# Optimization experiments

Hardware: AMD Instinct MI355X
Metric: run time of the kernel (lower is better)

The kernel has to match this reference:

```python
import jax, jax.numpy as jnp
import numpy as np
from jax import lax

H = 16        # linear_num_key_heads == linear_num_value_heads
DK = 64       # linear_key_head_dim
DV = 128      # linear_value_head_dim
HID = 2048    # hidden_size
KCONV = 4     # linear_conv_kernel_dim
SEQ = 2048
KEY_DIM = H * DK       # 1024
VAL_DIM = H * DV       # 2048
CONV_DIM = 2 * KEY_DIM + VAL_DIM  # 4096


def _l2norm(x, eps=1e-6):
    return x * lax.rsqrt(jnp.sum(x * x, axis=-1, keepdims=True) + eps)


def setup_inputs() -> dict:
    key = jax.random.key(0)
    ks = jax.random.split(key, 10)
    s = 0.02
    return {
        "hidden_states": jax.random.normal(ks[0], (1, SEQ, HID), jnp.float32),
        "in_proj_qkv": jax.random.normal(ks[1], (CONV_DIM, HID), jnp.float32) * s,
        "in_proj_a": jax.random.normal(ks[2], (H, HID), jnp.float32) * s,
        "in_proj_b": jax.random.normal(ks[3], (H, HID), jnp.float32) * s,
        "in_proj_z": jax.random.normal(ks[4], (VAL_DIM, HID), jnp.float32) * s,
        "conv_w": jax.random.normal(ks[5], (CONV_DIM, 1, KCONV), jnp.float32) * 0.5,
        "A_log": jax.random.normal(ks[6], (H,), jnp.float32) * 0.5,
        "dt_bias": jnp.ones((H,), jnp.float32),
        "norm_w": jnp.ones((DV,), jnp.float32),
        "out_proj": jax.random.normal(ks[7], (HID, VAL_DIM), jnp.float32) * s,
        "is_prefill": 1,
    }


def reference(hidden_states, in_proj_qkv, in_proj_a, in_proj_b, in_proj_z,
              conv_w, A_log, dt_bias, norm_w, out_proj, is_prefill):
    b, s, _ = hidden_states.shape  # b == 1
    # QKV projection: (1, S, CONV_DIM)
    mixed = jnp.einsum('bsh,oh->bso', hidden_states, in_proj_qkv)
    # Depthwise causal conv1d over time (left pad K-1), then SiLU
    x = mixed.transpose(0, 2, 1)  # (1, C, S)
    x = lax.conv_general_dilated(
        x, conv_w, window_strides=(1,), padding=[(KCONV - 1, 0)],
        feature_group_count=CONV_DIM, dimension_numbers=('NCH', 'OIH', 'NCH'))
    mixed = jax.nn.silu(x).transpose(0, 2, 1)[0]  # (S, CONV_DIM), squeeze batch

    q = mixed[:, :KEY_DIM].reshape(s, H, DK)
    k = mixed[:, KEY_DIM:2 * KEY_DIM].reshape(s, H, DK)
    v = mixed[:, 2 * KEY_DIM:].reshape(s, H, DV)

    hs = hidden_states[0]  # (S, HID)
    a = hs @ in_proj_a.T                      # (S, H)
    g = -jnp.exp(A_log) * jax.nn.softplus(a + dt_bias)  # (S, H) log-decay
    beta = jax.nn.sigmoid(hs @ in_proj_b.T)   # (S, H)
    z = (hs @ in_proj_z.T).reshape(s, H, DV)  # (S, H, DV)

    q = _l2norm(q) * (1.0 / np.sqrt(DK))
    k = _l2norm(k)

    # Delta-rule recurrence; prefill -> zero initial state
    S0 = jnp.zeros((H, DK, DV), jnp.float32)

    def step(St, inp):
        q_t, k_t, v_t, g_t, beta_t = inp
        St = St * jnp.exp(g_t)[:, None, None]            # decay
        kv_mem = jnp.einsum('hk,hkv->hv', k_t, St)       # read
        delta = (v_t - kv_mem) * beta_t[:, None]         # gated error
        St = St + jnp.einsum('hk,hv->hkv', k_t, delta)   # rank-1 update
        o_t = jnp.einsum('hk,hkv->hv', q_t, St)          # query read
        return St, o_t

    _, core = lax.scan(step, S0, (q, k, v, g, beta))  # core: (S, H, DV)

    # Gated RMSNorm over DV, then SiLU(z) gate
    var = jnp.mean(core * core, axis=-1, keepdims=True)
    core = core * lax.rsqrt(var + 1e-6) * norm_w
    core = core * jax.nn.silu(z)
    core = core.reshape(1, s, VAL_DIM)
    return jnp.einsum('bsv,hv->bsh', core, out_proj)
```

## Files before the change

kernel.cpp:

```cpp
#include <hip/hip_runtime.h>
#include <stdint.h>


#define SEQ 2048
#define HIDDEN 2048
#define NH 16
#define DKv 64
#define DVv 128
#define KEY_DIM 1024
#define VAL_DIM 2048
#define CONV_DIM 4096

typedef __bf16 bf16;
typedef unsigned short u16;
typedef __attribute__((ext_vector_type(8))) __bf16 bf16x8;
typedef __attribute__((ext_vector_type(4))) __bf16 bf16x4;
typedef __attribute__((ext_vector_type(4))) float f32x4;

#define AS1 __attribute__((address_space(1)))
#define AS3 __attribute__((address_space(3)))
#define GLDS16(src, dst) __builtin_amdgcn_global_load_lds((AS1 const void*)(src), (AS3 void*)(dst), 16, 0, 0)

__device__ __forceinline__ float b2f(u16 u) {
  union { unsigned int i; float f; } c; c.i = ((unsigned int)u) << 16; return c.f;
}
__device__ __forceinline__ float sigmoidf_(float x) { return 1.0f / (1.0f + __expf(-x)); }

__global__ void detect_dtype(const u16* __restrict__ p, unsigned* __restrict__ flag) {
  int lane = threadIdx.x;
  int cnt = 0;
  for (int w = lane; w < 2048; w += 64) {
    unsigned e = (p[2 * w] >> 7) & 0xFF;
    if (e < 64) cnt++;
  }
  cnt += __shfl_xor(cnt, 1);  cnt += __shfl_xor(cnt, 2);  cnt += __shfl_xor(cnt, 4);
  cnt += __shfl_xor(cnt, 8);  cnt += __shfl_xor(cnt, 16); cnt += __shfl_xor(cnt, 32);
  if (lane == 0) *flag = (cnt > 64) ? 1u : 0u;
}

__global__ __launch_bounds__(256)
void cvt_bf16(const void* __restrict__ src, bf16* __restrict__ dst, long n,
              const unsigned* __restrict__ flagp) {
  long i = ((long)blockIdx.x * 256 + threadIdx.x) * 8;
  if (i >= n) return;
  if (*flagp) {
    const f32x4* s = (const f32x4*)((const float*)src + i);
    f32x4 a = s[0], b = s[1];
    bf16x8 o;
#pragma unroll
    for (int j = 0; j < 4; ++j) { o[j] = (bf16)a[j]; o[4 + j] = (bf16)b[j]; }
    *(bf16x8*)(dst + i) = o;
  } else {
    *(bf16x8*)(dst + i) = *(const bf16x8*)((const bf16*)src + i);
  }
}

template<bool F32OUT>
__global__ __launch_bounds__(256, 2)
void gemm_nt(const void* __restrict__ Araw, const void* __restrict__ Braw,
             void* __restrict__ Cv, int N, int K,
             const unsigned* __restrict__ flagp, int useA, int useB) {
  __shared__ __align__(16) bf16 As[128 * 32];
  __shared__ __align__(16) bf16 Bs[128 * 32];
  const bool f32g = (*flagp != 0);
  const bool fA = useA && f32g;
  const bool fB = useB && f32g;
  const int tid  = threadIdx.x;
  const int lane = tid & 63;
  const int wv   = tid >> 6;
  const int wm   = (wv & 1) << 6;
  const int wn   = (wv >> 1) << 6;
  const long bm  = (long)blockIdx.y * 128;
  const long bn  = (long)blockIdx.x * 128;

  f32x4 acc[4][4] = {};

  for (int k0 = 0; k0 < K; k0 += 32) {
#pragma unroll
    for (int it = 0; it < 2; ++it) {
      int e   = (it * 256 + tid) * 8;
      int row = e >> 5;
      int col = e & 31;
      long offA = (bm + row) * (long)K + (k0 + col);
      long offB = (bn + row) * (long)K + (k0 + col);
      if (fA) {
        const float* g = (const float*)Araw + offA;
        f32x4 u0 = *(const f32x4*)g, u1 = *(const f32x4*)(g + 4);
        bf16x8 bv;
#pragma unroll
        for (int j = 0; j < 4; ++j) { bv[j] = (bf16)u0[j]; bv[4 + j] = (bf16)u1[j]; }
        *(bf16x8*)&As[e] = bv;
      } else {
        const bf16* g = (const bf16*)Araw + offA;
        GLDS16(g, &As[e]);
      }
      if (fB) {
        const float* g = (const float*)Braw + offB;
        f32x4 u0 = *(const f32x4*)g, u1 = *(const f32x4*)(g + 4);
        bf16x8 bv;
#pragma unroll
        for (int j = 0; j < 4; ++j) { bv[j] = (bf16)u0[j]; bv[4 + j] = (bf16)u1[j]; }
        *(bf16x8*)&Bs[e] = bv;
      } else {
        const bf16* g = (const bf16*)Braw + offB;
        GLDS16(g, &Bs[e]);
      }
    }
    __syncthreads();

    const bf16x8* As8 = (const bf16x8*)As;
    const bf16x8* Bs8 = (const bf16x8*)Bs;
    const int r = lane & 15, q = lane >> 4;
    bf16x8 af[4], bfr[4];
#pragma unroll
    for (int i = 0; i < 4; ++i) af[i]  = As8[(wm + i * 16 + r) * 4 + q];
#pragma unroll
    for (int j = 0; j < 4; ++j) bfr[j] = Bs8[(wn + j * 16 + r) * 4 + q];
#pragma unroll
    for (int i = 0; i < 4; ++i)
#pragma unroll
      for (int j = 0; j < 4; ++j)
        acc[i][j] = __builtin_amdgcn_mfma_f32_16x16x32_bf16(af[i], bfr[j], acc[i][j], 0, 0, 0);
    __syncthreads();
  }

  const int r = lane & 15, q = lane >> 4;
#pragma unroll
  for (int i = 0; i < 4; ++i)
#pragma unroll
    for (int j = 0; j < 4; ++j) {
      long row = bm + wm + i * 16 + q * 4;
      long col = bn + wn + j * 16 + r;
#pragma unroll
      for (int rr = 0; rr < 4; ++rr) {
        if constexpr (F32OUT) ((float*)Cv)[(row + rr) * N + col] = acc[i][j][rr];
        else                  ((bf16*)Cv)[(row + rr) * N + col] = (bf16)acc[i][j][rr];
      }
    }
}

__device__ void gemm_body_bf16(char* smemc, const bf16* __restrict__ A,
                               const bf16* __restrict__ B, bf16* __restrict__ C,
                               int N, int K, int bx, int by, int tid) {
  bf16* As = (bf16*)smemc;
  bf16* Bs = (bf16*)(smemc + 8192);
  const int lane = tid & 63;
  const int wv = tid >> 6, wm = (wv & 1) << 6, wn = (wv >> 1) << 6;
  const long bm = (long)by * 128, bn = (long)bx * 128;
  f32x4 acc[4][4] = {};
  for (int k0 = 0; k0 < K; k0 += 32) {
#pragma unroll
    for (int it = 0; it < 2; ++it) {
      int e = (it * 256 + tid) * 8;
      int row = e >> 5, col = e & 31;
      const bf16* gA = A + (bm + row) * (long)K + k0 + col;
      const bf16* gB = B + (bn + row) * (long)K + k0 + col;
      GLDS16(gA, &As[e]);
      GLDS16(gB, &Bs[e]);
    }
    __syncthreads();
    const bf16x8* As8 = (const bf16x8*)As;
    const bf16x8* Bs8 = (const bf16x8*)Bs;
    const int r = lane & 15, q = lane >> 4;
    bf16x8 af[4], bfr[4];
#pragma unroll
    for (int i = 0; i < 4; ++i) af[i]  = As8[(wm + i * 16 + r) * 4 + q];
#pragma unroll
    for (int j = 0; j < 4; ++j) bfr[j] = Bs8[(wn + j * 16 + r) * 4 + q];
#pragma unroll
    for (int i = 0; i < 4; ++i)
#pragma unroll
      for (int j = 0; j < 4; ++j)
        acc[i][j] = __builtin_amdgcn_mfma_f32_16x16x32_bf16(af[i], bfr[j], acc[i][j], 0, 0, 0);
    __syncthreads();
  }
  const int r = lane & 15, q = lane >> 4;
#pragma unroll
  for (int i = 0; i < 4; ++i)
#pragma unroll
    for (int j = 0; j < 4; ++j) {
      long row = bm + wm + i * 16 + q * 4;
      long col = bn + wn + j * 16 + r;
#pragma unroll
      for (int rr = 0; rr < 4; ++rr)
        C[(row + rr) * (long)N + col] = (bf16)acc[i][j][rr];
    }
}

__global__ __launch_bounds__(256)
void proj_ab(const void* __restrict__ hsr, const void* __restrict__ War,
             const void* __restrict__ Wbr, const void* __restrict__ A_logr,
             const void* __restrict__ dtbr,
             float* __restrict__ eg, float* __restrict__ bet,
             float* __restrict__ gb,
             const unsigned* __restrict__ flagp) {
  const bool f32g = (*flagp != 0);
  const int t  = threadIdx.x;
  const int sl = t >> 5;
  const int o  = t & 31;
  const int h  = o & 15;
  const long s = (long)blockIdx.x * 8 + sl;
  float a0 = 0.f, a1 = 0.f, a2 = 0.f, a3 = 0.f;
  if (f32g) {
    const f32x4* x4 = (const f32x4*)((const float*)hsr + s * HIDDEN);
    const f32x4* w4 = (const f32x4*)((const float*)((o < 16) ? War : Wbr) + (long)h * HIDDEN);
#pragma unroll 8
    for (int k4 = 0; k4 < 512; ++k4) {
      f32x4 xv = x4[k4], wv = w4[k4];
      a0 = fmaf(xv[0], wv[0], a0);
      a1 = fmaf(xv[1], wv[1], a1);
      a2 = fmaf(xv[2], wv[2], a2);
      a3 = fmaf(xv[3], wv[3], a3);
    }
  } else {
    const bf16x8* x8 = (const bf16x8*)((const bf16*)hsr + s * HIDDEN);
    const bf16x8* w8 = (const bf16x8*)((const bf16*)((o < 16) ? War : Wbr) + (long)h * HIDDEN);
#pragma unroll 8
    for (int k8 = 0; k8 < 256; ++k8) {
      bf16x8 xv = x8[k8], wv = w8[k8];
      a0 += (float)xv[0] * (float)wv[0] + (float)xv[4] * (float)wv[4];
      a1 += (float)xv[1] * (float)wv[1] + (float)xv[5] * (float)wv[5];
      a2 += (float)xv[2] * (float)wv[2] + (float)xv[6] * (float)wv[6];
      a3 += (float)xv[3] * (float)wv[3] + (float)xv[7] * (float)wv[7];
    }
  }
  const float a = (a0 + a1) + (a2 + a3);
  if (o < 16) {
    float alog = f32g ? ((const float*)A_logr)[h] : b2f(((const u16*)A_logr)[h]);
    float dtb  = f32g ? ((const float*)dtbr)[h]   : b2f(((const u16*)dtbr)[h]);
    float xx = a + dtb;
    float sp = fmaxf(xx, 0.f) + log1pf(__expf(-fabsf(xx)));
    float gg = -__expf(alog) * sp;
    if (gb) gb[s * NH + h] = gg;
    eg[s * NH + h] = __expf(gg);
  } else {
    bet[s * NH + h] = sigmoidf_(a);
  }
}

__global__ __launch_bounds__(256)
void conv_norm(const bf16* __restrict__ mixed, const void* __restrict__ convwr,
               bf16* __restrict__ qbuf, bf16* __restrict__ kbuf, bf16* __restrict__ vbuf,
               const unsigned* __restrict__ flagp) {
  const bool f32g = (*flagp != 0);
  const int s = blockIdx.x;
  const int c = blockIdx.y * 256 + threadIdx.x;
  float w0, w1, w2, w3;
  if (f32g) {
    const float* wp = (const float*)convwr + (long)c * 4;
    w0 = wp[0]; w1 = wp[1]; w2 = wp[2]; w3 = wp[3];
  } else {
    const u16* wp = (const u16*)convwr + (long)c * 4;
    w0 = b2f(wp[0]); w1 = b2f(wp[1]); w2 = b2f(wp[2]); w3 = b2f(wp[3]);
  }
  float acc = w3 * (float)mixed[(long)s * CONV_DIM + c];
  if (s >= 1) acc += w2 * (float)mixed[(long)(s - 1) * CONV_DIM + c];
  if (s >= 2) acc += w1 * (float)mixed[(long)(s - 2) * CONV_DIM + c];
  if (s >= 3) acc += w0 * (float)mixed[(long)(s - 3) * CONV_DIM + c];
  float y = acc * sigmoidf_(acc);
  if (c < 2 * KEY_DIM) {
    float ss = y * y;
    ss += __shfl_xor(ss, 1);  ss += __shfl_xor(ss, 2);  ss += __shfl_xor(ss, 4);
    ss += __shfl_xor(ss, 8);  ss += __shfl_xor(ss, 16); ss += __shfl_xor(ss, 32);
    float scale = rsqrtf(ss + 1e-6f);
    if (c < KEY_DIM) scale *= 0.125f;
    y *= scale;
  }
  if (c < KEY_DIM)            qbuf[(long)s * KEY_DIM + c] = (bf16)y;
  else if (c < 2 * KEY_DIM)   kbuf[(long)s * KEY_DIM + (c - KEY_DIM)] = (bf16)y;
  else                        vbuf[(long)s * VAL_DIM + (c - 2 * KEY_DIM)] = (bf16)y;
}

template<int CTRL>
__device__ __forceinline__ float dpp_add(float x) {
  int y = __builtin_amdgcn_update_dpp(0, __float_as_int(x), CTRL, 0xF, 0xF, true);
  return x + __int_as_float(y);
}
__device__ __forceinline__ float dpp_sum16(float x) {
  x = dpp_add<0xB1>(x);
  x = dpp_add<0x4E>(x);
  x = dpp_add<0x141>(x);
  x = dpp_add<0x140>(x);
  return x;
}

__global__ __launch_bounds__(256, 2)
void fused_scan(const bf16* __restrict__ qbuf, const bf16* __restrict__ kbuf,
                const bf16* __restrict__ vbuf, const float* __restrict__ eg,
                const float* __restrict__ bet, bf16* __restrict__ core,
                const bf16* __restrict__ hsb, const bf16* __restrict__ wzb,
                bf16* __restrict__ zbuf, const void* __restrict__ woutr,
                bf16* __restrict__ woutb, const unsigned* __restrict__ flagp,
                int nScan, int nGemm) {
  __shared__ __align__(16) char smem[16384];
  const int t = threadIdx.x;
  const int b = blockIdx.x;

  if (b < nScan) {
    const int h  = b >> 3;
    const int vg = (b & 7) * 16;
    const int g  = t >> 4;
    const int L  = t & 15;
    bf16*  kqs = (bf16*)smem;
    bf16*  vts = (bf16*)(smem + 8192);
    float* ets = (float*)(smem + 9216);
    float* bts = (float*)(smem + 9344);

#define STAGE(buf, s0)                                                          \
    {                                                                           \
      int byte = t * 16;                                                        \
      const bf16* src;                                                          \
      if (byte < 2048) {                                                        \
        int row = byte >> 7, el = (byte & 127) >> 1;                            \
        src = kbuf + (long)((s0) + row) * KEY_DIM + h * DKv + el;               \
      } else {                                                                  \
        int b2 = byte - 2048;                                                   \
        int row = b2 >> 7, el = (b2 & 127) >> 1;                                \
        src = qbuf + (long)((s0) + row) * KEY_DIM + h * DKv + el;               \
      }                                                                         \
      GLDS16(src, smem + (buf) * 4096 + byte);                                  \
      if (t < 32) {                                                             \
        int row = t >> 1, el = (t & 1) * 8;                                     \
        const bf16* vsrc = vbuf + (long)((s0) + row) * VAL_DIM + h * DVv + vg + el; \
        GLDS16(vsrc, smem + 8192 + (buf) * 512 + t * 16);                       \
      }                                                                         \
    }

    float er = 0.f, br = 0.f;
    if (t < 16)      er = eg[(long)t * NH + h];
    else if (t < 32) br = bet[(long)(t - 16) * NH + h];
    STAGE(0, 0);
    if (t < 16)      ets[t] = er;
    else if (t < 32) bts[t - 16] = br;
    __syncthreads();

    float S0 = 0.f, S1 = 0.f, S2 = 0.f, S3 = 0.f;
    for (int tile = 0; tile < 128; ++tile) {
      const int buf = tile & 1, nb = buf ^ 1;
      if (tile < 127) {
        STAGE(nb, (tile + 1) * 16);
        if (t < 16)      er = eg[(long)((tile + 1) * 16 + t) * NH + h];
        else if (t < 32) br = bet[(long)((tile + 1) * 16 + (t - 16)) * NH + h];
      }
      const bf16*  ktb = kqs + buf * 2048;
      const bf16*  qtb = ktb + 1024;
      const bf16*  vtb = vts + buf * 256;
      const float* etb = ets + buf * 16;
      const float* btb = bts + buf * 16;
      const long sbase = (long)tile * 16;

      bf16x4 kR[2], qR[2];
      float  vR[2], eR[2], bR[2];
      kR[0] = *(const bf16x4*)(ktb + 0 * 64 + L * 4);
      qR[0] = *(const bf16x4*)(qtb + 0 * 64 + L * 4);
      vR[0] = (float)vtb[0 * 16 + g];  eR[0] = etb[0];  bR[0] = btb[0];
      kR[1] = *(const bf16x4*)(ktb + 1 * 64 + L * 4);
      qR[1] = *(const bf16x4*)(qtb + 1 * 64 + L * 4);
      vR[1] = (float)vtb[1 * 16 + g];  eR[1] = etb[1];  bR[1] = btb[1];
#pragma unroll
      for (int s = 0; s < 16; ++s) {
        const int sl = s & 1;
        bf16x4 kk = kR[sl], qq = qR[sl];
        float vv = vR[sl], ee = eR[sl], bb = bR[sl];
        if (s < 14) {
          const int s2 = s + 2;
          kR[sl] = *(const bf16x4*)(ktb + s2 * 64 + L * 4);
          qR[sl] = *(const bf16x4*)(qtb + s2 * 64 + L * 4);
          vR[sl] = (float)vtb[s2 * 16 + g];
          eR[sl] = etb[s2];  bR[sl] = btb[s2];
        }
        float ebt = ee * bb, vbt = vv * bb;
        float k0 = (float)kk[0], k1 = (float)kk[1], k2 = (float)kk[2], k3 = (float)kk[3];
        float D0 = S0 * ee, D1 = S1 * ee, D2 = S2 * ee, D3 = S3 * ee;
        float p = (k0 * S0 + k1 * S1) + (k2 * S2 + k3 * S3);
        p = dpp_sum16(p);
        float delta = vbt - ebt * p;
        S0 = fmaf(k0, delta, D0); S1 = fmaf(k1, delta, D1);
        S2 = fmaf(k2, delta, D2); S3 = fmaf(k3, delta, D3);
        float q0 = (float)qq[0], q1 = (float)qq[1], q2 = (float)qq[2], q3 = (float)qq[3];
        float o = (q0 * S0 + q1 * S1) + (q2 * S2 + q3 * S3);
        o = dpp_sum16(o);
        if (L == 0) core[(sbase + s) * VAL_DIM + h * DVv + vg + g] = (bf16)o;
      }
      if (tile < 127) {
        if (t < 16)      ets[nb * 16 + t] = er;
        else if (t < 32) bts[nb * 16 + (t - 16)] = br;
      }
      __syncthreads();
    }
#undef STAGE
  } else if (b < nScan + nGemm) {
    int gb = b - nScan;
    gemm_body_bf16(smem, hsb, wzb, zbuf, VAL_DIM, HIDDEN, gb & 15, gb >> 4, t);
  } else {
    long i = ((long)(b - nScan - nGemm) * 256 + t) * 8;
    if (i < (long)HIDDEN * VAL_DIM) {
      if (*flagp) {
        const f32x4* s = (const f32x4*)((const float*)woutr + i);
        f32x4 a = s[0], c = s[1];
        bf16x8 o;
#pragma unroll
        for (int j = 0; j < 4; ++j) { o[j] = (bf16)a[j]; o[4 + j] = (bf16)c[j]; }
        *(bf16x8*)(woutb + i) = o;
      } else {
        *(bf16x8*)(woutb + i) = *(const bf16x8*)((const bf16*)woutr + i);
      }
    }
  }
}


__global__ __launch_bounds__(256, 2)
void chunk_a(const bf16* __restrict__ kbuf, const bf16* __restrict__ vbuf,
             const float* __restrict__ gbuf, const float* __restrict__ betp,
             bf16* __restrict__ dlocT, bf16* __restrict__ whig, bf16* __restrict__ wlog,
             const bf16* __restrict__ hsb, const bf16* __restrict__ wzb,
             bf16* __restrict__ zbuf, const void* __restrict__ woutr,
             bf16* __restrict__ woutb, const unsigned* __restrict__ flagp) {
  __shared__ __align__(16) char smem[25600];
  const int t = threadIdx.x;
  const int b = blockIdx.x;
  if (b < 512) {
    const int c = b >> 4, h = b & 15;
    bf16*  Ks   = (bf16*)smem;
    float* At   = (float*)(smem + 8192);
    float* cumS = (float*)(smem + 24576);
    float* bS   = (float*)(smem + 24832);
    float* dS   = (float*)(smem + 25088);
#pragma unroll
    for (int it = 0; it < 2; ++it) {
      int byte = (it * 256 + t) * 16;
      int row = byte >> 7, col = (byte & 127) >> 1;
      const bf16* src = kbuf + (long)(c * 64 + row) * KEY_DIM + h * DKv + col;
      GLDS16(src, smem + byte);
    }
    if (t < 64) {
      float cc = gbuf[(long)(c * 64 + t) * NH + h];
#pragma unroll
      for (int d = 1; d < 64; d <<= 1) { float y = __shfl_up(cc, d); if (t >= d) cc += y; }
      cumS[t] = cc;
      dS[t] = __expf(cc);
      bS[t] = betp[(long)(c * 64 + t) * NH + h];
    }
    {
      f32x4 z = {0.f, 0.f, 0.f, 0.f};
#pragma unroll
      for (int i = 0; i < 4; ++i) ((f32x4*)At)[t * 4 + i] = z;
    }
    __syncthreads();
    {
      const int lane = t & 63, wv = t >> 6;
      const int r = lane & 15, q = lane >> 4;
      const bf16x8* Ks8 = (const bf16x8*)Ks;
#pragma unroll
      for (int n = 0; n < 4; ++n) {
        f32x4 acc = {0.f, 0.f, 0.f, 0.f};
#pragma unroll
        for (int kk = 0; kk < 2; ++kk) {
          bf16x8 af  = Ks8[(wv * 16 + r) * 8 + kk * 4 + q];
          bf16x8 bfv = Ks8[(n  * 16 + r) * 8 + kk * 4 + q];
          acc = __builtin_amdgcn_mfma_f32_16x16x32_bf16(af, bfv, acc, 0, 0, 0);
        }
        const int i = n * 16 + r;
#pragma unroll
        for (int rr = 0; rr < 4; ++rr) {
          const int tr = wv * 16 + q * 4 + rr;
          if (i < tr)
            At[i * 64 + tr] = bS[tr] * __expf(cumS[tr] - cumS[i]) * acc[rr];
        }
      }
    }
    __syncthreads();
    if (t < 192) {
      float x[64];
      const long ch = (long)(c * 16 + h);
      if (t < 128) {
#pragma unroll
        for (int s = 0; s < 64; ++s)
          x[s] = bS[s] * (float)vbuf[(long)(c * 64 + s) * VAL_DIM + h * DVv + t];
      } else {
        const int k = t - 128;
#pragma unroll
        for (int s = 0; s < 64; ++s)
          x[s] = bS[s] * dS[s] * (float)Ks[s * 64 + k];
      }
#pragma unroll
      for (int s = 0; s < 64; ++s) {
        const float val = x[s];
        const f32x4* row4 = (const f32x4*)(At + s * 64);
#pragma unroll
        for (int qd = (s >> 2); qd < 16; ++qd) {
          f32x4 a4 = row4[qd];
          x[qd * 4 + 0] = fmaf(-a4[0], val, x[qd * 4 + 0]);
          x[qd * 4 + 1] = fmaf(-a4[1], val, x[qd * 4 + 1]);
          x[qd * 4 + 2] = fmaf(-a4[2], val, x[qd * 4 + 2]);
          x[qd * 4 + 3] = fmaf(-a4[3], val, x[qd * 4 + 3]);
        }
      }
      if (t < 128) {
        bf16* dp = dlocT + ch * 8192 + (long)t * 64;
#pragma unroll
        for (int s4 = 0; s4 < 16; ++s4) {
          bf16x4 o;
          o[0] = (bf16)x[s4 * 4 + 0]; o[1] = (bf16)x[s4 * 4 + 1];
          o[2] = (bf16)x[s4 * 4 + 2]; o[3] = (bf16)x[s4 * 4 + 3];
          *(bf16x4*)(dp + s4 * 4) = o;
        }
      } else {
        const int k = t - 128;
        const long wb = ch * 4096;
#pragma unroll
        for (int s = 0; s < 64; ++s) {
          float v = -x[s];
          bf16 hh = (bf16)v;
          whig[wb + s * 64 + k] = hh;
          wlog[wb + s * 64 + k] = (bf16)(v - (float)hh);
        }
      }
    }
  } else if (b < 768) {
    int gb = b - 512;
    gemm_body_bf16(smem, hsb, wzb, zbuf, VAL_DIM, HIDDEN, gb & 15, gb >> 4, t);
  } else {
    long i = ((long)(b - 768) * 256 + t) * 8;
    if (i < (long)HIDDEN * VAL_DIM) {
      if (*flagp) {
        const f32x4* s = (const f32x4*)((const float*)woutr + i);
        f32x4 a = s[0], cc = s[1];
        bf16x8 o;
#pragma unroll
        for (int j = 0; j < 4; ++j) { o[j] = (bf16)a[j]; o[4 + j] = (bf16)cc[j]; }
        *(bf16x8*)(woutb + i) = o;
      } else {
        *(bf16x8*)(woutb + i) = *(const bf16x8*)((const bf16*)woutr + i);
      }
    }
  }
}

__global__ __launch_bounds__(256, 1)
void chunk_b(const bf16* __restrict__ qbuf, const bf16* __restrict__ kbuf,
             const float* __restrict__ gbuf, const bf16* __restrict__ dlocT,
             const bf16* __restrict__ whig, const bf16* __restrict__ wlog,
             bf16* __restrict__ dTg, bf16* __restrict__ o1g) {
  __shared__ __align__(16) char smem[114688];
  bf16* Wh  = (bf16*)(smem);
  bf16* Wl  = (bf16*)(smem + 16384);
  bf16* Qs  = (bf16*)(smem + 32768);
  bf16* Ks  = (bf16*)(smem + 49152);
  bf16* Dls = (bf16*)(smem + 65536);
  bf16* KT  = (bf16*)(smem + 73728);
  bf16* Shi = (bf16*)(smem + 81920);
  bf16* Slo = (bf16*)(smem + 86016);
  bf16* Dth = (bf16*)(smem + 90112);
  bf16* Dtl = (bf16*)(smem + 94208);
  float* fSa = (float*)(smem + 98304);
  float* dSa = (float*)(smem + 106496);

  const int t = threadIdx.x;
  const int h = blockIdx.x >> 2, vq = blockIdx.x & 3;
  const int lane = t & 63, w = t >> 6;
  const int r = lane & 15, q = lane >> 4;
  const int tb = w * 16 + q * 4;

  auto stage = [&](int bb, int cc) {
    const long c16h = (long)(cc * 16 + h);
#pragma unroll
    for (int it = 0; it < 2; ++it) {
      int p = it * 256 + t;
      int row = p >> 3, g = p & 7;
      int sg = ((g ^ (row & 7)) << 3);
      GLDS16(whig + c16h * 4096 + row * 64 + sg, (char*)Wh + bb * 8192 + p * 16);
      GLDS16(wlog + c16h * 4096 + row * 64 + sg, (char*)Wl + bb * 8192 + p * 16);
      GLDS16(qbuf + (long)(cc * 64 + row) * KEY_DIM + h * DKv + sg, (char*)Qs + bb * 8192 + p * 16);
      GLDS16(kbuf + (long)(cc * 64 + row) * KEY_DIM + h * DKv + (g << 3), (char*)Ks + bb * 8192 + p * 16);
    }
    {
      int row = t >> 3, g = t & 7;
      int sg = ((g ^ (row & 7)) << 3);
      GLDS16(dlocT + c16h * 8192 + (long)(vq * 32 + row) * 64 + sg,
             (char*)Dls + bb * 4096 + t * 16);
    }
  };

  {
    float g8[8];
#pragma unroll
    for (int i = 0; i < 8; ++i)
      g8[i] = gbuf[(long)((w * 8 + i) * 64 + lane) * NH + h];
#pragma unroll
    for (int i = 0; i < 8; ++i) {
      float cs = g8[i];
#pragma unroll
      for (int d = 1; d < 64; d <<= 1) { float y = __shfl_up(cs, d); if (lane >= d) cs += y; }
      float tot = __shfl(cs, 63);
      fSa[(w * 8 + i) * 64 + lane] = __expf(tot - cs);
      dSa[(w * 8 + i) * 64 + lane] = __expf(cs);
    }
  }
  {
    f32x4 z = {0.f, 0.f, 0.f, 0.f};
    ((f32x4*)Shi)[t] = z;
    ((f32x4*)Slo)[t] = z;
  }
  stage(0, 0);
  f32x4 Sacc[2] = {};

  const int va = w & 1, kt0 = (w >> 1) * 2;

  for (int c = 0; c < 32; ++c) {
    const int buf = c & 1, nb = buf ^ 1;
    __syncthreads();
    if (c < 31) stage(nb, c + 1);
    const bf16* wh = Wh + buf * 4096;
    const bf16* wl = Wl + buf * 4096;
    const bf16* qs = Qs + buf * 4096;
    const bf16* ks = Ks + buf * 4096;
    const bf16* dls = Dls + buf * 2048;
    const float* fS = fSa + c * 64;
    const float* dS = dSa + c * 64;
    const long gch = (long)(c * 16 + h) * 8192 + (long)(vq * 32) * 64;

    if (c < 31) {
      const int k2 = lane;
#pragma unroll
      for (int ii = 0; ii < 16; ++ii) {
        const int i = w * 16 + ii;
        const int pg = (i >> 3) ^ (k2 & 7);
        KT[k2 * 64 + pg * 8 + (i & 7)] = ks[i * 64 + k2];
      }
    }

    float fs4[4], ds4[4];
#pragma unroll
    for (int rr = 0; rr < 4; ++rr) { fs4[rr] = fS[tb + rr]; ds4[rr] = dS[tb + rr]; }

    bf16x8 wahi[2], walo[2], qa[2];
#pragma unroll
    for (int kk = 0; kk < 2; ++kk) {
      const int row = w * 16 + r;
      const int g = (kk * 4 + q) ^ (row & 7);
      wahi[kk] = *(const bf16x8*)(wh + row * 64 + g * 8);
      walo[kk] = *(const bf16x8*)(wl + row * 64 + g * 8);
      qa[kk]   = *(const bf16x8*)(qs + row * 64 + g * 8);
    }
    bf16x8 sh[2][2], sl[2][2];
#pragma unroll
    for (int n = 0; n < 2; ++n)
#pragma unroll
      for (int kk = 0; kk < 2; ++kk) {
        const int vrow = n * 16 + r;
        const int g = (kk * 4 + q) ^ (vrow & 7);
        sh[n][kk] = *(const bf16x8*)(Shi + vrow * 64 + g * 8);
        sl[n][kk] = *(const bf16x8*)(Slo + vrow * 64 + g * 8);
      }
    float dl4[2][4];
#pragma unroll
    for (int n = 0; n < 2; ++n) {
      const int vloc = n * 16 + r;
      const int pg = (tb >> 3) ^ (vloc & 7);
      bf16x4 dv4 = *(const bf16x4*)(dls + vloc * 64 + pg * 8 + (tb & 7));
#pragma unroll
      for (int rr = 0; rr < 4; ++rr) dl4[n][rr] = (float)dv4[rr];
    }

    f32x4 da[2] = {}, oa[2] = {};
#pragma unroll
    for (int n = 0; n < 2; ++n)
#pragma unroll
      for (int kk = 0; kk < 2; ++kk) {
        da[n] = __builtin_amdgcn_mfma_f32_16x16x32_bf16(wahi[kk], sh[n][kk], da[n], 0, 0, 0);
        da[n] = __builtin_amdgcn_mfma_f32_16x16x32_bf16(wahi[kk], sl[n][kk], da[n], 0, 0, 0);
        da[n] = __builtin_amdgcn_mfma_f32_16x16x32_bf16(walo[kk], sh[n][kk], da[n], 0, 0, 0);
        oa[n] = __builtin_amdgcn_mfma_f32_16x16x32_bf16(qa[kk],   sh[n][kk], oa[n], 0, 0, 0);
        oa[n] = __builtin_amdgcn_mfma_f32_16x16x32_bf16(qa[kk],   sl[n][kk], oa[n], 0, 0, 0);
      }

#pragma unroll
    for (int n = 0; n < 2; ++n) {
      const int vloc = n * 16 + r;
      bf16x4 dpk, opk, fhk, flk;
#pragma unroll
      for (int rr = 0; rr < 4; ++rr) {
        float dv = dl4[n][rr] + da[n][rr];
        dpk[rr] = (bf16)dv;
        float p = fs4[rr] * dv;
        bf16 ph = (bf16)p;
        fhk[rr] = ph;
        flk[rr] = (bf16)(p - (float)ph);
        opk[rr] = (bf16)(ds4[rr] * oa[n][rr]);
      }
      *(bf16x4*)(dTg + gch + (long)vloc * 64 + tb) = dpk;
      *(bf16x4*)(o1g + gch + (long)vloc * 64 + tb) = opk;
      const int pg = (tb >> 3) ^ (vloc & 7);
      *(bf16x4*)(Dth + vloc * 64 + pg * 8 + (tb & 7)) = fhk;
      *(bf16x4*)(Dtl + vloc * 64 + pg * 8 + (tb & 7)) = flk;
    }

    asm volatile("s_waitcnt lgkmcnt(0)" ::: "memory");
    __builtin_amdgcn_sched_barrier(0);
    __builtin_amdgcn_s_barrier();
    __builtin_amdgcn_sched_barrier(0);

    if (c < 31) {
      const float dC = dS[63];
      bf16x8 dh[2], dlo2[2], ktf[2][2];
#pragma unroll
      for (int kk = 0; kk < 2; ++kk) {
        const int vrow = va * 16 + r;
        const int g = (kk * 4 + q) ^ (vrow & 7);
        dh[kk]   = *(const bf16x8*)(Dth + vrow * 64 + g * 8);
        dlo2[kk] = *(const bf16x8*)(Dtl + vrow * 64 + g * 8);
      }
#pragma unroll
      for (int m = 0; m < 2; ++m)
#pragma unroll
        for (int kk = 0; kk < 2; ++kk) {
          const int krow = (kt0 + m) * 16 + r;
          const int g = (kk * 4 + q) ^ (krow & 7);
          ktf[m][kk] = *(const bf16x8*)(KT + krow * 64 + g * 8);
        }
#pragma unroll
      for (int m = 0; m < 2; ++m) {
        f32x4 sa;
#pragma unroll
        for (int rr = 0; rr < 4; ++rr) sa[rr] = dC * Sacc[m][rr];
#pragma unroll
        for (int kk = 0; kk < 2; ++kk) {
          sa = __builtin_amdgcn_mfma_f32_16x16x32_bf16(dh[kk],   ktf[m][kk], sa, 0, 0, 0);
          sa = __builtin_amdgcn_mfma_f32_16x16x32_bf16(dlo2[kk], ktf[m][kk], sa, 0, 0, 0);
        }
        Sacc[m] = sa;
        const int k = (kt0 + m) * 16 + r;
#pragma unroll
        for (int rr = 0; rr < 4; ++rr) {
          const int v = va * 16 + q * 4 + rr;
          float s = sa[rr];
          bf16 hh = (bf16)s;
          const int pg = (k >> 3) ^ (v & 7);
          Shi[v * 64 + pg * 8 + (k & 7)] = hh;
          Slo[v * 64 + pg * 8 + (k & 7)] = (bf16)(s - (float)hh);
        }
      }
    }
  }
}

__global__ __launch_bounds__(256, 2)
void chunk_c(const bf16* __restrict__ qbuf, const bf16* __restrict__ kbuf,
             const float* __restrict__ gbuf, const bf16* __restrict__ dTg,
             const bf16* __restrict__ o1g, bf16* __restrict__ core) {
  __shared__ __align__(16) char smem[57600];
  const int t = threadIdx.x;
  const int c = blockIdx.x >> 4, h = blockIdx.x & 15;
  const long c16h = (long)(c * 16 + h);
  bf16* Qs  = (bf16*)smem;
  bf16* Ksl = (bf16*)(smem + 8192);
  bf16* Pl  = (bf16*)(smem + 16384);
  const bf16* dT  = (const bf16*)(smem + 24576);
  const bf16* o1l = (const bf16*)(smem + 40960);
  float* cumS = (float*)(smem + 57344);

#pragma unroll
  for (int it = 0; it < 2; ++it) {
    int byte = (it * 256 + t) * 16;
    int row = byte >> 7, col = (byte & 127) >> 1;
    GLDS16(qbuf + (long)(c * 64 + row) * KEY_DIM + h * DKv + col, smem + byte);
    GLDS16(kbuf + (long)(c * 64 + row) * KEY_DIM + h * DKv + col, smem + 8192 + byte);
  }
#pragma unroll
  for (int it = 0; it < 4; ++it) {
    int byte = (it * 256 + t) * 16;
    GLDS16(dTg + c16h * 8192 + (byte >> 1), smem + 24576 + byte);
    GLDS16(o1g + c16h * 8192 + (byte >> 1), smem + 40960 + byte);
  }
  if (t < 64) {
    float cc = gbuf[(long)(c * 64 + t) * NH + h];
#pragma unroll
    for (int d = 1; d < 64; d <<= 1) { float y = __shfl_up(cc, d); if (t >= d) cc += y; }
    cumS[t] = cc;
  }
  __syncthreads();

  const int lane = t & 63, wv = t >> 6;
  const int r = lane & 15, q = lane >> 4;
  const bf16x8* Qs8 = (const bf16x8*)Qs;
  const bf16x8* Ks8 = (const bf16x8*)Ksl;

#pragma unroll
  for (int n = 0; n < 4; ++n) {
    f32x4 acc = {0.f, 0.f, 0.f, 0.f};
#pragma unroll
    for (int kk = 0; kk < 2; ++kk)
      acc = __builtin_amdgcn_mfma_f32_16x16x32_bf16(
          Qs8[(wv * 16 + r) * 8 + kk * 4 + q], Ks8[(n * 16 + r) * 8 + kk * 4 + q], acc, 0, 0, 0);
    const int i = n * 16 + r;
#pragma unroll
    for (int rr = 0; rr < 4; ++rr) {
      const int tr = wv * 16 + q * 4 + rr;
      Pl[tr * 64 + i] = (i <= tr) ? (bf16)(__expf(cumS[tr] - cumS[i]) * acc[rr]) : (bf16)0.0f;
    }
  }
  __syncthreads();

  {
    const bf16x8* Pl8 = (const bf16x8*)Pl;
    const bf16x8* dT8 = (const bf16x8*)dT;
    bf16x8 pf[2];
#pragma unroll
    for (int kk = 0; kk < 2; ++kk) pf[kk] = Pl8[(wv * 16 + r) * 8 + kk * 4 + q];
#pragma unroll
    for (int n = 0; n < 8; ++n) {
      const int v = n * 16 + r;
      f32x4 acc;
#pragma unroll
      for (int rr = 0; rr < 4; ++rr)
        acc[rr] = (float)o1l[v * 64 + (wv * 16 + q * 4 + rr)];
#pragma unroll
      for (int kk = 0; kk < 2; ++kk)
        acc = __builtin_amdgcn_mfma_f32_16x16x32_bf16(
            pf[kk], dT8[(n * 16 + r) * 8 + kk * 4 + q], acc, 0, 0, 0);
#pragma unroll
      for (int rr = 0; rr < 4; ++rr) {
        const int tr = wv * 16 + q * 4 + rr;
        core[(long)(c * 64 + tr) * VAL_DIM + h * DVv + v] = (bf16)acc[rr];
      }
    }
  }
}

__global__ __launch_bounds__(256)
void gate_norm(const bf16* __restrict__ core, const bf16* __restrict__ zb,
               const void* __restrict__ normwr, bf16* __restrict__ gated,
               const unsigned* __restrict__ flagp) {
  const bool f32g = (*flagp != 0);
  const int s  = blockIdx.x;
  const int t  = threadIdx.x;
  const int h  = t >> 4;
  const int li = t & 15;
  const long base = (long)s * VAL_DIM + h * DVv + li * 8;
  bf16x8 c8 = *(const bf16x8*)(core + base);
  bf16x8 z8 = *(const bf16x8*)(zb + base);
  float x[8], z[8], nw[8];
  float ss = 0.f;
#pragma unroll
  for (int j = 0; j < 8; ++j) { x[j] = (float)c8[j]; z[j] = (float)z8[j]; ss += x[j] * x[j]; }
  if (f32g) {
    const float* np_ = (const float*)normwr + li * 8;
#pragma unroll
    for (int j = 0; j < 8; ++j) nw[j] = np_[j];
  } else {
    const u16* np_ = (const u16*)normwr + li * 8;
#pragma unroll
    for (int j = 0; j < 8; ++j) nw[j] = b2f(np_[j]);
  }
  ss += __shfl_xor(ss, 1); ss += __shfl_xor(ss, 2);
  ss += __shfl_xor(ss, 4); ss += __shfl_xor(ss, 8);
  float scale = rsqrtf(ss * (1.f / 128.f) + 1e-6f);
#pragma unroll
  for (int j = 0; j < 8; ++j) {
    float y = x[j] * scale * nw[j];
    y *= z[j] * sigmoidf_(z[j]);
    gated[base + j] = (bf16)y;
  }
}

extern "C" void kernel_launch(void* const* d_in, const int* in_sizes, int n_in,
                              void* d_out, int out_size, void* d_ws, size_t ws_size,
                              hipStream_t stream) {
  char* ws = (char*)d_ws;
  const bool big = ws_size >= ((48u << 20) + (512u << 10));

  if (big) {
    bf16*  hsb   = (bf16*)ws;
    bf16*  wqkvb = (bf16*)(ws + (8u << 20));
    bf16*  wzb   = (bf16*)(ws + (8u << 20));
    bf16*  zbuf  = (bf16*)(ws + (16u << 20));
    bf16*  mixed = (bf16*)(ws + (24u << 20));
    bf16*  whig  = (bf16*)(ws + (24u << 20));
    bf16*  wlog  = (bf16*)(ws + (28u << 20));
    bf16*  woutb = (bf16*)(ws + (32u << 20));
    bf16*  qbuf  = (bf16*)(ws + (40u << 20));
    bf16*  kbuf  = (bf16*)(ws + (44u << 20));
    bf16*  gated = (bf16*)(ws + (40u << 20));
    bf16*  dTg   = (bf16*)ws;
    bf16*  o1g   = (bf16*)(ws + (8u << 20));
    float* egp  = (float*)(ws + (48u << 20));
    float* betp = (float*)(ws + (48u << 20) + (128u << 10));
    float* gbp  = (float*)(ws + (48u << 20) + (256u << 10));
    unsigned* flagp = (unsigned*)(ws + (48u << 20) + (384u << 10));
    bf16* vbuf  = (bf16*)d_out;
    bf16* dlocp = (bf16*)((char*)d_out + (8u << 20));
    bf16* corep = (bf16*)d_out;

    detect_dtype<<<1, 64, 0, stream>>>((const u16*)d_in[0], flagp);
    proj_ab<<<SEQ / 8, 256, 0, stream>>>(d_in[0], d_in[2], d_in[3], d_in[6], d_in[7], egp, betp, gbp, flagp);
    cvt_bf16<<<(SEQ * HIDDEN) / 2048, 256, 0, stream>>>(d_in[0], hsb, (long)SEQ * HIDDEN, flagp);
    cvt_bf16<<<(CONV_DIM * HIDDEN) / 2048, 256, 0, stream>>>(d_in[1], wqkvb, (long)CONV_DIM * HIDDEN, flagp);
    gemm_nt<false><<<dim3(CONV_DIM / 128, SEQ / 128), 256, 0, stream>>>(hsb, wqkvb, mixed, CONV_DIM, HIDDEN, flagp, 0, 0);
    cvt_bf16<<<(VAL_DIM * HIDDEN) / 2048, 256, 0, stream>>>(d_in[4], wzb, (long)VAL_DIM * HIDDEN, flagp);
    conv_norm<<<dim3(SEQ, CONV_DIM / 256), 256, 0, stream>>>(mixed, d_in[5], qbuf, kbuf, vbuf, flagp);
    chunk_a<<<512 + 256 + 2048, 256, 0, stream>>>(kbuf, vbuf, gbp, betp, dlocp, whig, wlog,
                                                  hsb, wzb, zbuf, d_in[9], woutb, flagp);
    chunk_b<<<64, 256, 0, stream>>>(qbuf, kbuf, gbp, dlocp, whig, wlog, dTg, o1g);
    chunk_c<<<512, 256, 0, stream>>>(qbuf, kbuf, gbp, dTg, o1g, corep);
    gate_norm<<<SEQ, 256, 0, stream>>>(corep, zbuf, d_in[8], gated, flagp);
    gemm_nt<true><<<dim3(HIDDEN / 128, SEQ / 128), 256, 0, stream>>>(gated, woutb, d_out, HIDDEN, VAL_DIM, flagp, 0, 0);
  } else {
    bf16* mixed = (bf16*)ws;
    bf16* qbuf  = (bf16*)(ws + (16u << 20));
    bf16* kbuf  = (bf16*)(ws + (20u << 20));
    bf16* zbuf  = (bf16*)ws;
    bf16* corep = (bf16*)(ws + (8u << 20));
    bf16* gated = (bf16*)(ws + (16u << 20));
    float* egp  = (float*)(ws + (24u << 20));
    float* betp = (float*)(ws + (24u << 20) + (128u << 10));
    unsigned* flagp = (unsigned*)(ws + (24u << 20) + (256u << 10));
    bf16* vbuf  = (bf16*)d_out;

    detect_dtype<<<1, 64, 0, stream>>>((const u16*)d_in[0], flagp);
    proj_ab<<<SEQ / 8, 256, 0, stream>>>(d_in[0], d_in[2], d_in[3], d_in[6], d_in[7], egp, betp, nullptr, flagp);
    gemm_nt<false><<<dim3(CONV_DIM / 128, SEQ / 128), 256, 0, stream>>>(d_in[0], d_in[1], mixed, CONV_DIM, HIDDEN, flagp, 1, 1);
    conv_norm<<<dim3(SEQ, CONV_DIM / 256), 256, 0, stream>>>(mixed, d_in[5], qbuf, kbuf, vbuf, flagp);
    gemm_nt<false><<<dim3(VAL_DIM / 128, SEQ / 128), 256, 0, stream>>>(d_in[0], d_in[4], zbuf, VAL_DIM, HIDDEN, flagp, 1, 1);
    fused_scan<<<128, 256, 0, stream>>>(qbuf, kbuf, vbuf, egp, betp, corep,
                                        nullptr, nullptr, nullptr, nullptr, nullptr, flagp,
                                        128, 0);
    gate_norm<<<SEQ, 256, 0, stream>>>(corep, zbuf, d_in[8], gated, flagp);
    gemm_nt<true><<<dim3(HIDDEN / 128, SEQ / 128), 256, 0, stream>>>(gated, d_in[9], d_out, HIDDEN, VAL_DIM, flagp, 0, 1);
  }
}
```

Measured before the change: 499.2 us.

## Fuse QKV and Z projections into one double-buffered GEMM and remap workspace

Concatenates the QKV and Z weight matrices in the workspace and runs a single GEMM over both, writing each half to its own output buffer. The Z GEMM that was packed into chunk_a is removed from it. gemm_nt gains a two-stage LDS double buffer so the next K tile loads while the current one is multiplied. The workspace layout is reshuffled to fit the combined weight buffer, which creates aliasing risks (for example mixed now lives in d_out and vbuf at the start of ws, on top of hsb).

```diff
diff --git a/kernel.cpp b/kernel.cpp
--- a/kernel.cpp
+++ b/kernel.cpp
@@ -60,8 +60,8 @@
 void gemm_nt(const void* __restrict__ Araw, const void* __restrict__ Braw,
              void* __restrict__ Cv, int N, int K,
              const unsigned* __restrict__ flagp, int useA, int useB) {
-  __shared__ __align__(16) bf16 As[128 * 32];
-  __shared__ __align__(16) bf16 Bs[128 * 32];
+  __shared__ __align__(16) bf16 As[2][128 * 32];
+  __shared__ __align__(16) bf16 Bs[2][128 * 32];
   const bool f32g = (*flagp != 0);
   const bool fA = useA && f32g;
   const bool fB = useB && f32g;
@@ -75,7 +75,7 @@
 
   f32x4 acc[4][4] = {};
 
-  for (int k0 = 0; k0 < K; k0 += 32) {
+  auto stage = [&](int bb, int k0) {
 #pragma unroll
     for (int it = 0; it < 2; ++it) {
       int e   = (it * 256 + tid) * 8;
@@ -89,10 +89,9 @@
         bf16x8 bv;
 #pragma unroll
         for (int j = 0; j < 4; ++j) { bv[j] = (bf16)u0[j]; bv[4 + j] = (bf16)u1[j]; }
-        *(bf16x8*)&As[e] = bv;
+        *(bf16x8*)&As[bb][e] = bv;
       } else {
-        const bf16* g = (const bf16*)Araw + offA;
-        GLDS16(g, &As[e]);
+        GLDS16((const bf16*)Araw + offA, &As[bb][e]);
       }
       if (fB) {
         const float* g = (const float*)Braw + offB;
@@ -100,17 +99,22 @@
         bf16x8 bv;
 #pragma unroll
         for (int j = 0; j < 4; ++j) { bv[j] = (bf16)u0[j]; bv[4 + j] = (bf16)u1[j]; }
-        *(bf16x8*)&Bs[e] = bv;
+        *(bf16x8*)&Bs[bb][e] = bv;
       } else {
-        const bf16* g = (const bf16*)Braw + offB;
-        GLDS16(g, &Bs[e]);
-      }
-    }
-    __syncthreads();
-
-    const bf16x8* As8 = (const bf16x8*)As;
-    const bf16x8* Bs8 = (const bf16x8*)Bs;
-    const int r = lane & 15, q = lane >> 4;
+        GLDS16((const bf16*)Braw + offB, &Bs[bb][e]);
+      }
+    }
+  };
+
+  stage(0, 0);
+  __syncthreads();
+  int buf = 0;
+  const int r = lane & 15, q = lane >> 4;
+  const int nk = K >> 5;
+  for (int ks = 0; ks < nk; ++ks) {
+    if (ks + 1 < nk) stage(buf ^ 1, (ks + 1) * 32);
+    const bf16x8* As8 = (const bf16x8*)As[buf];
+    const bf16x8* Bs8 = (const bf16x8*)Bs[buf];
     bf16x8 af[4], bfr[4];
 #pragma unroll
     for (int i = 0; i < 4; ++i) af[i]  = As8[(wm + i * 16 + r) * 4 + q];
@@ -122,9 +126,9 @@
       for (int j = 0; j < 4; ++j)
         acc[i][j] = __builtin_amdgcn_mfma_f32_16x16x32_bf16(af[i], bfr[j], acc[i][j], 0, 0, 0);
     __syncthreads();
-  }
-
-  const int r = lane & 15, q = lane >> 4;
+    buf ^= 1;
+  }
+
 #pragma unroll
   for (int i = 0; i < 4; ++i)
 #pragma unroll
@@ -136,6 +140,71 @@
         if constexpr (F32OUT) ((float*)Cv)[(row + rr) * N + col] = acc[i][j][rr];
         else                  ((bf16*)Cv)[(row + rr) * N + col] = (bf16)acc[i][j][rr];
       }
+    }
+}
+
+__global__ __launch_bounds__(256, 2)
+void gemm_qkvz(const bf16* __restrict__ A, const bf16* __restrict__ B,
+               bf16* __restrict__ Cmixed, bf16* __restrict__ Cz) {
+  __shared__ __align__(16) bf16 As[2][128 * 32];
+  __shared__ __align__(16) bf16 Bs[2][128 * 32];
+  const int tid  = threadIdx.x;
+  const int lane = tid & 63;
+  const int wv   = tid >> 6;
+  const int wm   = (wv & 1) << 6;
+  const int wn   = (wv >> 1) << 6;
+  const long bm  = (long)blockIdx.y * 128;
+  const long bn  = (long)blockIdx.x * 128;
+  const int K = HIDDEN;
+
+  f32x4 acc[4][4] = {};
+
+  auto stage = [&](int bb, int k0) {
+#pragma unroll
+    for (int it = 0; it < 2; ++it) {
+      int e = (it * 256 + tid) * 8;
+      int row = e >> 5, col = e & 31;
+      GLDS16(A + (bm + row) * (long)K + k0 + col, &As[bb][e]);
+      GLDS16(B + (bn + row) * (long)K + k0 + col, &Bs[bb][e]);
+    }
+  };
+
+  stage(0, 0);
+  __syncthreads();
+  int buf = 0;
+  const int r = lane & 15, q = lane >> 4;
+  const int nk = K >> 5;
+  for (int ks = 0; ks < nk; ++ks) {
+    if (ks + 1 < nk) stage(buf ^ 1, (ks + 1) * 32);
+    const bf16x8* As8 = (const bf16x8*)As[buf];
+    const bf16x8* Bs8 = (const bf16x8*)Bs[buf];
+    bf16x8 af[4], bfr[4];
+#pragma unroll
+    for (int i = 0; i < 4; ++i) af[i]  = As8[(wm + i * 16 + r) * 4 + q];
+#pragma unroll
+    for (int j = 0; j < 4; ++j) bfr[j] = Bs8[(wn + j * 16 + r) * 4 + q];
+#pragma unroll
+    for (int i = 0; i < 4; ++i)
+#pragma unroll
+      for (int j = 0; j < 4; ++j)
+        acc[i][j] = __builtin_amdgcn_mfma_f32_16x16x32_bf16(af[i], bfr[j], acc[i][j], 0, 0, 0);
+    __syncthreads();
+    buf ^= 1;
+  }
+
+  const bool isz = (bn >= 4096);
+  bf16* Cp = isz ? Cz : Cmixed;
+  const long cstride = isz ? 2048 : 4096;
+  const long cb = (isz ? (bn - 4096) : bn) + wn;
+#pragma unroll
+  for (int i = 0; i < 4; ++i)
+#pragma unroll
+    for (int j = 0; j < 4; ++j) {
+      long row = bm + wm + i * 16 + q * 4;
+      long col = cb + j * 16 + r;
+#pragma unroll
+      for (int rr = 0; rr < 4; ++rr)
+        Cp[(row + rr) * cstride + col] = (bf16)acc[i][j][rr];
     }
 }
 
@@ -414,9 +483,8 @@
 void chunk_a(const bf16* __restrict__ kbuf, const bf16* __restrict__ vbuf,
              const float* __restrict__ gbuf, const float* __restrict__ betp,
              bf16* __restrict__ dlocT, bf16* __restrict__ whig, bf16* __restrict__ wlog,
-             const bf16* __restrict__ hsb, const bf16* __restrict__ wzb,
-             bf16* __restrict__ zbuf, const void* __restrict__ woutr,
-             bf16* __restrict__ woutb, const unsigned* __restrict__ flagp) {
+             const void* __restrict__ woutr, bf16* __restrict__ woutb,
+             const unsigned* __restrict__ flagp) {
   __shared__ __align__(16) char smem[25600];
   const int t = threadIdx.x;
   const int b = blockIdx.x;
@@ -518,11 +586,8 @@
         }
       }
     }
-  } else if (b < 768) {
-    int gb = b - 512;
-    gemm_body_bf16(smem, hsb, wzb, zbuf, VAL_DIM, HIDDEN, gb & 15, gb >> 4, t);
   } else {
-    long i = ((long)(b - 768) * 256 + t) * 8;
+    long i = ((long)(b - 512) * 256 + t) * 8;
     if (i < (long)HIDDEN * VAL_DIM) {
       if (*flagp) {
         const f32x4* s = (const f32x4*)((const float*)woutr + i);
@@ -873,35 +938,35 @@
 
   if (big) {
     bf16*  hsb   = (bf16*)ws;
-    bf16*  wqkvb = (bf16*)(ws + (8u << 20));
-    bf16*  wzb   = (bf16*)(ws + (8u << 20));
-    bf16*  zbuf  = (bf16*)(ws + (16u << 20));
-    bf16*  mixed = (bf16*)(ws + (24u << 20));
+    bf16*  wcomb = (bf16*)(ws + (8u << 20));
+    bf16*  wzpart= (bf16*)(ws + (24u << 20));
+    bf16*  zbuf  = (bf16*)(ws + (32u << 20));
+    bf16*  mixed = (bf16*)d_out;
+    bf16*  vbuf  = (bf16*)ws;
+    bf16*  qbuf  = (bf16*)(ws + (40u << 20));
+    bf16*  kbuf  = (bf16*)(ws + (44u << 20));
     bf16*  whig  = (bf16*)(ws + (24u << 20));
     bf16*  wlog  = (bf16*)(ws + (28u << 20));
-    bf16*  woutb = (bf16*)(ws + (32u << 20));
-    bf16*  qbuf  = (bf16*)(ws + (40u << 20));
-    bf16*  kbuf  = (bf16*)(ws + (44u << 20));
+    bf16*  woutb = (bf16*)(ws + (8u << 20));
+    bf16*  dlocp = (bf16*)((char*)d_out + (8u << 20));
+    bf16*  dTg   = (bf16*)ws;
+    bf16*  o1g   = (bf16*)(ws + (16u << 20));
+    bf16*  corep = (bf16*)d_out;
     bf16*  gated = (bf16*)(ws + (40u << 20));
-    bf16*  dTg   = (bf16*)ws;
-    bf16*  o1g   = (bf16*)(ws + (8u << 20));
     float* egp  = (float*)(ws + (48u << 20));
     float* betp = (float*)(ws + (48u << 20) + (128u << 10));
     float* gbp  = (float*)(ws + (48u << 20) + (256u << 10));
     unsigned* flagp = (unsigned*)(ws + (48u << 20) + (384u << 10));
-    bf16* vbuf  = (bf16*)d_out;
-    bf16* dlocp = (bf16*)((char*)d_out + (8u << 20));
-    bf16* corep = (bf16*)d_out;
 
     detect_dtype<<<1, 64, 0, stream>>>((const u16*)d_in[0], flagp);
     proj_ab<<<SEQ / 8, 256, 0, stream>>>(d_in[0], d_in[2], d_in[3], d_in[6], d_in[7], egp, betp, gbp, flagp);
     cvt_bf16<<<(SEQ * HIDDEN) / 2048, 256, 0, stream>>>(d_in[0], hsb, (long)SEQ * HIDDEN, flagp);
-    cvt_bf16<<<(CONV_DIM * HIDDEN) / 2048, 256, 0, stream>>>(d_in[1], wqkvb, (long)CONV_DIM * HIDDEN, flagp);
-    gemm_nt<false><<<dim3(CONV_DIM / 128, SEQ / 128), 256, 0, stream>>>(hsb, wqkvb, mixed, CONV_DIM, HIDDEN, flagp, 0, 0);
-    cvt_bf16<<<(VAL_DIM * HIDDEN) / 2048, 256, 0, stream>>>(d_in[4], wzb, (long)VAL_DIM * HIDDEN, flagp);
+    cvt_bf16<<<(CONV_DIM * HIDDEN) / 2048, 256, 0, stream>>>(d_in[1], wcomb, (long)CONV_DIM * HIDDEN, flagp);
+    cvt_bf16<<<(VAL_DIM * HIDDEN) / 2048, 256, 0, stream>>>(d_in[4], wzpart, (long)VAL_DIM * HIDDEN, flagp);
+    gemm_qkvz<<<dim3((CONV_DIM + VAL_DIM) / 128, SEQ / 128), 256, 0, stream>>>(hsb, wcomb, mixed, zbuf);
     conv_norm<<<dim3(SEQ, CONV_DIM / 256), 256, 0, stream>>>(mixed, d_in[5], qbuf, kbuf, vbuf, flagp);
-    chunk_a<<<512 + 256 + 2048, 256, 0, stream>>>(kbuf, vbuf, gbp, betp, dlocp, whig, wlog,
-                                                  hsb, wzb, zbuf, d_in[9], woutb, flagp);
+    chunk_a<<<512 + 2048, 256, 0, stream>>>(kbuf, vbuf, gbp, betp, dlocp, whig, wlog,
+                                            d_in[9], woutb, flagp);
     chunk_b<<<64, 256, 0, stream>>>(qbuf, kbuf, gbp, dlocp, whig, wlog, dTg, o1g);
     chunk_c<<<512, 256, 0, stream>>>(qbuf, kbuf, gbp, dTg, o1g, corep);
     gate_norm<<<SEQ, 256, 0, stream>>>(corep, zbuf, d_in[8], gated, flagp);
```

After: 475.4 us. 1.05x faster.
